# Kernel optimization log

Measured on AMD Instinct MI355X. Metric: run time of the kernel, lower is better.

The kernel has to match this reference:

```python
import jax, jax.numpy as jnp
import numpy as np
import math

N_HEAD = 16
N_EMBD = 1024
HEAD_DIM = N_EMBD // N_HEAD
B, T = 2, 2048


def setup_inputs() -> dict:
    key = jax.random.key(0)
    k1, k2, k3 = jax.random.split(key, 3)
    scale = 0.02
    x = jax.random.normal(k1, (B, T, N_EMBD), dtype=jnp.float32)
    W_attn = jax.random.normal(k2, (N_EMBD, 3 * N_EMBD), dtype=jnp.float32) * scale
    b_attn = jnp.zeros((3 * N_EMBD,), dtype=jnp.float32)
    W_proj = jax.random.normal(k3, (N_EMBD, N_EMBD), dtype=jnp.float32) * scale
    b_proj = jnp.zeros((N_EMBD,), dtype=jnp.float32)
    return {"x": x, "W_attn": W_attn, "b_attn": b_attn, "W_proj": W_proj, "b_proj": b_proj}


def reference(x, W_attn, b_attn, W_proj, b_proj):
    b, t, c = x.shape
    qkv = x @ W_attn + b_attn                      # [B,T,3C]
    q, k, v = jnp.split(qkv, 3, axis=-1)
    # [B,T,C] -> [B,H,T,D]
    def heads(z):
        return z.reshape(b, t, N_HEAD, HEAD_DIM).transpose(0, 2, 1, 3)
    q, k, v = heads(q), heads(k), heads(v)
    att = jnp.einsum('bhqd,bhkd->bhqk', q, k) * (1.0 / math.sqrt(HEAD_DIM))
    causal = jnp.tril(jnp.ones((t, t), dtype=bool))  # [T,T]
    att = jnp.where(causal[None, None], att, -jnp.inf)
    att = jax.nn.softmax(att, axis=-1)
    y = jnp.einsum('bhqk,bhkd->bhqd', att, v)      # [B,H,T,D]
    y = y.transpose(0, 2, 1, 3).reshape(b, t, c)   # [B,T,C]
    return y @ W_proj + b_proj
```

## Files before the change

### kernel.cpp

```cpp
#include <hip/hip_runtime.h>
#include <hip/hip_bf16.h>


typedef __bf16 bf16_t;
typedef __bf16 bf16x8 __attribute__((ext_vector_type(8)));
typedef float f32x4 __attribute__((ext_vector_type(4)));
typedef unsigned short ushort_t;

#define QSCALE 0.18033688011f

__device__ __forceinline__ void glds16(const bf16_t* g, ushort_t* l) {
  __builtin_amdgcn_global_load_lds(
      (const __attribute__((address_space(1))) unsigned int*)g,
      (__attribute__((address_space(3))) unsigned int*)l, 16, 0, 0);
}

__global__ __launch_bounds__(256) void prep_kernel(
    const float* __restrict__ x, const float* __restrict__ W_attn,
    const float* __restrict__ W_proj, ushort_t* __restrict__ Xb,
    ushort_t* __restrict__ WtA, ushort_t* __restrict__ WtP) {
  const int bid = blockIdx.x, tid = threadIdx.x;
  if (bid < 4096) {
    int i = bid * 256 + tid;
    float4 v = ((const float4*)x)[i];
    ushort4 o;
    o.x = __builtin_bit_cast(unsigned short, (bf16_t)v.x);
    o.y = __builtin_bit_cast(unsigned short, (bf16_t)v.y);
    o.z = __builtin_bit_cast(unsigned short, (bf16_t)v.z);
    o.w = __builtin_bit_cast(unsigned short, (bf16_t)v.w);
    ((ushort4*)Xb)[i] = o;
    return;
  }
  __shared__ ushort_t tile[32][33];
  const float* in;
  ushort_t* out;
  int C, bx, by;
  if (bid < 4096 + 3072) { int idx = bid - 4096; in = W_attn; out = WtA; C = 3072; bx = idx % 96; by = idx / 96; }
  else                   { int idx = bid - 7168; in = W_proj; out = WtP; C = 1024; bx = idx % 32; by = idx / 32; }
  const int tx = tid & 31, ty = tid >> 5;
  int cbase = bx * 32, rbase = by * 32;
#pragma unroll
  for (int i = ty; i < 32; i += 8)
    tile[i][tx] = __builtin_bit_cast(
        unsigned short, (bf16_t)in[(size_t)(rbase + i) * C + cbase + tx]);
  __syncthreads();
#pragma unroll
  for (int i = ty; i < 32; i += 8)
    out[(size_t)(cbase + i) * 1024 + rbase + tx] = tile[tx][i];
}

__global__ __launch_bounds__(512) void qkv_gemm_kernel(
    const bf16_t* __restrict__ X, const bf16_t* __restrict__ WtA,
    const float* __restrict__ bias, bf16_t* __restrict__ Qd,
    bf16_t* __restrict__ Kd, bf16_t* __restrict__ Vtd) {
  __shared__ ushort_t As[2 * 256 * 32];
  __shared__ ushort_t Bs[2 * 192 * 32];
  const int tid  = threadIdx.x;
  const int lane = tid & 63, wave = tid >> 6;
  const int l15  = lane & 15, quad = lane >> 4;
  const int wrow = (wave >> 1) * 64;
  const int wcol = (wave & 1) * 96;
  const int mtile = blockIdx.x * 256, ntile = blockIdx.y * 192;
  const int K = 1024;
  const int lr4 = lane >> 2;
  const int csw = ((lane & 3) ^ ((lr4 >> 1) & 3)) * 8;
  const int rsw = (quad ^ ((l15 >> 1) & 3)) * 8;
  const bf16_t* Xrow = X   + (size_t)(mtile + lr4) * K + csw;
  const bf16_t* Wrow = WtA + (size_t)(ntile + lr4) * K + csw;

#define STAGE_QKV(kb, Asl, Bsl)                                              \
  {                                                                          \
    _Pragma("unroll")                                                        \
    for (int kk = 0; kk < 4; kk++) {                                         \
      int s = wave + kk * 8;                                                 \
      if (s < 16)      glds16(Xrow + (size_t)(s * 16) * K + (kb), (Asl) + s * 512); \
      else if (s < 28) glds16(Wrow + (size_t)((s - 16) * 16) * K + (kb), (Bsl) + (s - 16) * 512); \
    }                                                                        \
  }

  f32x4 acc[4][6] = {};
  STAGE_QKV(0, As, Bs);
  __syncthreads();
  for (int kt = 0; kt < 32; kt++) {
    const int cur = kt & 1, nxt = cur ^ 1;
    if (kt + 1 < 32)
      STAGE_QKV((kt + 1) * 32, As + nxt * 8192, Bs + nxt * 6144);
    bf16x8 af[4], bfr[6];
#pragma unroll
    for (int i = 0; i < 4; i++)
      af[i] = *(const bf16x8*)&As[cur * 8192 + (wrow + i * 16 + l15) * 32 + rsw];
#pragma unroll
    for (int j = 0; j < 6; j++)
      bfr[j] = *(const bf16x8*)&Bs[cur * 6144 + (wcol + j * 16 + l15) * 32 + rsw];
#pragma unroll
    for (int i = 0; i < 4; i++)
#pragma unroll
      for (int j = 0; j < 6; j++)
        acc[i][j] = __builtin_amdgcn_mfma_f32_16x16x32_bf16(af[i], bfr[j], acc[i][j], 0, 0, 0);
    __syncthreads();
  }
#undef STAGE_QKV

  const int b = mtile >> 11;
#pragma unroll
  for (int j = 0; j < 6; j++) {
    int n = ntile + wcol + j * 16 + l15;
    float bv = bias[n];
    int sec = n >> 10, cc = n & 1023, h = cc >> 6, d = cc & 63;
    size_t bh = (size_t)(b * 16 + h);
    if (sec == 2) {
#pragma unroll
      for (int i = 0; i < 4; i++) {
        int tperm = (mtile & 2047) + wrow + ((i >> 1) << 5) + (quad << 3) + ((i & 1) << 2);
        ushort4 o4;
        o4.x = __builtin_bit_cast(unsigned short, (bf16_t)(acc[i][j][0] + bv));
        o4.y = __builtin_bit_cast(unsigned short, (bf16_t)(acc[i][j][1] + bv));
        o4.z = __builtin_bit_cast(unsigned short, (bf16_t)(acc[i][j][2] + bv));
        o4.w = __builtin_bit_cast(unsigned short, (bf16_t)(acc[i][j][3] + bv));
        *(ushort4*)&Vtd[(bh * 64 + d) * 2048 + tperm] = o4;
      }
    } else {
      const float sv = (sec == 0) ? QSCALE : 1.0f;
      bf16_t* Od = (sec == 0) ? Qd : Kd;
#pragma unroll
      for (int i = 0; i < 4; i++) {
#pragma unroll
        for (int r = 0; r < 4; r++) {
          int t = (mtile & 2047) + wrow + i * 16 + quad * 4 + r;
          Od[(bh * 2048 + t) * 64 + d] = (bf16_t)((acc[i][j][r] + bv) * sv);
        }
      }
    }
  }
}

__global__ __launch_bounds__(512) void attn_kernel(
    const bf16_t* __restrict__ Q, const bf16_t* __restrict__ K,
    const bf16_t* __restrict__ Vt, bf16_t* __restrict__ Y) {
  __shared__ ushort_t Ks[2][4096];
  __shared__ ushort_t Vs[2][4096];
  const int bh = blockIdx.y;
  const int qt = (blockIdx.y < 16) ? (15 - (int)blockIdx.x) : (int)blockIdx.x;
  const int tid = threadIdx.x, wave = tid >> 6, lane = tid & 63;
  const int l15 = lane & 15, quad = lane >> 4;
  const bf16_t* Qh = Q + (size_t)bh * 2048 * 64;
  const bf16_t* Kh = K + (size_t)bh * 2048 * 64;
  const bf16_t* Vh = Vt + (size_t)bh * 64 * 2048;
  const int b = bh >> 4, h = bh & 15;
  const int qw = qt * 128 + wave * 16;
  const int nkt = 2 * qt + 2;

  bf16x8 qa[2];
#pragma unroll
  for (int kc = 0; kc < 2; kc++)
    qa[kc] = *(const bf16x8*)(Qh + (size_t)(qw + l15) * 64 + kc * 32 + quad * 8);

  f32x4 o[4] = {};
  float lp = 0.f;
  const int rsw = (quad ^ ((l15 >> 1) & 3)) * 8;

  const int lr4 = lane >> 2;
  const int csw = ((lane & 3) ^ ((lr4 >> 1) & 3)) * 8;
  const bool isK = wave < 4;
  const int sw = isK ? wave : wave - 4;
  const int rbase = (sw & 1) * 32;
  const bf16_t* gp0;
  size_t rowstep;
  if (isK) { gp0 = Kh + (size_t)(rbase + lr4) * 64 + (sw >> 1) * 32 + csw;  rowstep = 64; }
  else     { gp0 = Vh + (size_t)(rbase + lr4) * 2048 + (sw >> 1) * 32 + csw; rowstep = 2048; }
  const size_t kstep = isK ? (size_t)64 * 64 : 64;
  ushort_t* dst0 = (isK ? Ks[0] : Vs[0]) + (sw >> 1) * 2048 + rbase * 32;
  ushort_t* dst1 = (isK ? Ks[1] : Vs[1]) + (sw >> 1) * 2048 + rbase * 32;

#pragma unroll
  for (int c = 0; c < 2; c++)
    glds16(gp0 + (size_t)(c * 16) * rowstep, dst0 + c * 512);

  f32x4 zz = {0.f, 0.f, 0.f, 0.f};
  for (int kt = 0; kt < nkt; kt++) {
    const int cur = kt & 1;
    __syncthreads();
    if (kt + 1 < nkt) {
      ushort_t* nd = cur ? dst0 : dst1;
#pragma unroll
      for (int c = 0; c < 2; c++)
        glds16(gp0 + (size_t)(kt + 1) * kstep + (size_t)(c * 16) * rowstep, nd + c * 512);
    }
#pragma unroll
    for (int h32 = 0; h32 < 2; h32++) {
      const int kb32 = kt * 64 + h32 * 32;
      if (kb32 > qw + 15) break;
      bf16x8 kb[2][2];
#pragma unroll
      for (int bn = 0; bn < 2; bn++)
#pragma unroll
        for (int kc = 0; kc < 2; kc++)
          kb[bn][kc] = *(const bf16x8*)&Ks[cur][kc * 2048 + (h32 * 32 + bn * 16 + l15) * 32 + rsw];
      f32x4 s[2];
#pragma unroll
      for (int bn = 0; bn < 2; bn++) {
        f32x4 t0 = __builtin_amdgcn_mfma_f32_16x16x32_bf16(kb[bn][0], qa[0], zz, 0, 0, 0);
        s[bn] = __builtin_amdgcn_mfma_f32_16x16x32_bf16(kb[bn][1], qa[1], t0, 0, 0, 0);
      }
      const bool dg = (kb32 + 31 > qw);
      const int qrow = qw + l15;
      bf16x8 pa;
#pragma unroll
      for (int r = 0; r < 4; r++) {
        float v0 = s[0][r];
        float v1 = s[1][r];
        if (dg) {
          int k0 = kb32 + quad * 4 + r;
          if (k0 > qrow) v0 = -1e5f;
          if (k0 + 16 > qrow) v1 = -1e5f;
        }
        float p0 = __builtin_amdgcn_exp2f(v0);
        float p1 = __builtin_amdgcn_exp2f(v1);
        lp += p0 + p1;
        pa[r]     = (bf16_t)p0;
        pa[4 + r] = (bf16_t)p1;
      }
#pragma unroll
      for (int ns = 0; ns < 4; ns++) {
        bf16x8 vb = *(const bf16x8*)&Vs[cur][h32 * 2048 + (ns * 16 + l15) * 32 + rsw];
        o[ns] = __builtin_amdgcn_mfma_f32_16x16x32_bf16(pa, vb, o[ns], 0, 0, 0);
      }
    }
  }
  lp += __shfl_xor(lp, 16);
  lp += __shfl_xor(lp, 32);
  float inv_l = 1.0f / fmaxf(lp, 1e-30f);
#pragma unroll
  for (int r = 0; r < 4; r++) {
    float il = __shfl(inv_l, quad * 4 + r);
    int t = qw + quad * 4 + r;
#pragma unroll
    for (int ns = 0; ns < 4; ns++) {
      int c = h * 64 + ns * 16 + l15;
      Y[((size_t)(b * 2048 + t)) * 1024 + c] = (bf16_t)(o[ns][r] * il);
    }
  }
}

__global__ __launch_bounds__(256) void proj_gemm_kernel(
    const bf16_t* __restrict__ Yb, const bf16_t* __restrict__ WtP,
    const float* __restrict__ bias, float* __restrict__ out) {
  __shared__ ushort_t As[128 * 32];
  __shared__ ushort_t Bs[64 * 32];
  const int tid = threadIdx.x;
  const int lane = tid & 63, wave = tid >> 6;
  const int l15 = lane & 15, quad = lane >> 4;
  const int wrow = (wave >> 1) * 64, wcol = (wave & 1) * 32;
  const int mtile = blockIdx.x * 128, ntile = blockIdx.y * 64;
  const int K = 1024;
  const int lr = lane >> 2;
  const int lc = (((lane & 3) ^ ((lr >> 1) & 3)) * 8);
  const bf16_t* Ap = Yb + (size_t)(mtile + wave * 32 + lr) * K + lc;
  const bf16_t* Bp = WtP + (size_t)(ntile + wave * 16 + lr) * K + lc;
  const int rsw = (quad ^ ((l15 >> 1) & 3)) * 8;
  ushort_t* Asw = As + wave * 32 * 32;
  ushort_t* Bsw = Bs + wave * 16 * 32;
  f32x4 acc[4][2] = {};
  for (int kb = 0; kb < K; kb += 32) {
    __syncthreads();
    glds16(Ap + kb, Asw);
    glds16(Ap + (size_t)16 * K + kb, Asw + 16 * 32);
    glds16(Bp + kb, Bsw);
    __syncthreads();
    bf16x8 af[4], bfr[2];
#pragma unroll
    for (int i = 0; i < 4; i++)
      af[i] = *(const bf16x8*)&As[(wrow + i * 16 + l15) * 32 + rsw];
#pragma unroll
    for (int j = 0; j < 2; j++)
      bfr[j] = *(const bf16x8*)&Bs[(wcol + j * 16 + l15) * 32 + rsw];
#pragma unroll
    for (int i = 0; i < 4; i++)
#pragma unroll
      for (int j = 0; j < 2; j++)
        acc[i][j] = __builtin_amdgcn_mfma_f32_16x16x32_bf16(af[i], bfr[j], acc[i][j], 0, 0, 0);
  }
#pragma unroll
  for (int j = 0; j < 2; j++) {
    int n = ntile + wcol + j * 16 + l15;
    float bv = bias[n];
#pragma unroll
    for (int i = 0; i < 4; i++) {
#pragma unroll
      for (int r = 0; r < 4; r++) {
        int m = mtile + wrow + i * 16 + quad * 4 + r;
        out[(size_t)m * 1024 + n] = acc[i][j][r] + bv;
      }
    }
  }
}

extern "C" void kernel_launch(void* const* d_in, const int* in_sizes, int n_in,
                              void* d_out, int out_size, void* d_ws, size_t ws_size,
                              hipStream_t stream) {
  const float* x      = (const float*)d_in[0];
  const float* W_attn = (const float*)d_in[1];
  const float* b_attn = (const float*)d_in[2];
  const float* W_proj = (const float*)d_in[3];
  const float* b_proj = (const float*)d_in[4];
  float* out = (float*)d_out;

  bf16_t* ws  = (bf16_t*)d_ws;
  bf16_t* WtA = ws;
  bf16_t* WtP = WtA + (size_t)3072 * 1024;
  bf16_t* Xb  = WtP + (size_t)1024 * 1024;
  bf16_t* Qb  = Xb + (size_t)4194304;
  bf16_t* Kb  = Qb + (size_t)4194304;
  bf16_t* Vtb = Kb + (size_t)4194304;
  bf16_t* Yb  = Vtb + (size_t)4194304;

  prep_kernel<<<8192, 256, 0, stream>>>(x, W_attn, W_proj,
      (ushort_t*)Xb, (ushort_t*)WtA, (ushort_t*)WtP);
  qkv_gemm_kernel<<<dim3(16, 16), 512, 0, stream>>>(Xb, WtA, b_attn, Qb, Kb, Vtb);
  attn_kernel<<<dim3(16, 32), 512, 0, stream>>>(Qb, Kb, Vtb, Yb);
  proj_gemm_kernel<<<dim3(32, 16), 256, 0, stream>>>(Yb, WtP, b_proj, out);
}
```

Before: 173.2 us.

## Triple-buffer QKV GEMM LDS stages with partial vmcnt waits

The QKV projection GEMM moves from double to triple buffering of its LDS tiles, issuing loads two k-steps ahead. Explicit s_waitcnt vmcnt counts per wave replace the full __syncthreads drain, so only the oldest stage must land before each barrier. This should hide global-load latency better, at the cost of 50% more LDS per block, which may reduce occupancy. The hand-counted vmcnt values (4 for waves that issue four loads, 3 for those that issue three) must match exactly for correctness.

```diff
diff --git a/kernel.cpp b/kernel.cpp
--- a/kernel.cpp
+++ b/kernel.cpp
@@ -53,8 +53,8 @@
     const bf16_t* __restrict__ X, const bf16_t* __restrict__ WtA,
     const float* __restrict__ bias, bf16_t* __restrict__ Qd,
     bf16_t* __restrict__ Kd, bf16_t* __restrict__ Vtd) {
-  __shared__ ushort_t As[2 * 256 * 32];
-  __shared__ ushort_t Bs[2 * 192 * 32];
+  __shared__ ushort_t As[3 * 256 * 32];
+  __shared__ ushort_t Bs[3 * 192 * 32];
   const int tid  = threadIdx.x;
   const int lane = tid & 63, wave = tid >> 6;
   const int l15  = lane & 15, quad = lane >> 4;
@@ -68,36 +68,48 @@
   const bf16_t* Xrow = X   + (size_t)(mtile + lr4) * K + csw;
   const bf16_t* Wrow = WtA + (size_t)(ntile + lr4) * K + csw;
 
-#define STAGE_QKV(kb, Asl, Bsl)                                              \
+#define STAGE_QKV(kb, slot)                                                  \
   {                                                                          \
+    ushort_t* Asl = As + (slot) * 8192;                                      \
+    ushort_t* Bsl = Bs + (slot) * 6144;                                      \
     _Pragma("unroll")                                                        \
     for (int kk = 0; kk < 4; kk++) {                                         \
       int s = wave + kk * 8;                                                 \
-      if (s < 16)      glds16(Xrow + (size_t)(s * 16) * K + (kb), (Asl) + s * 512); \
-      else if (s < 28) glds16(Wrow + (size_t)((s - 16) * 16) * K + (kb), (Bsl) + (s - 16) * 512); \
+      if (s < 16)      glds16(Xrow + (size_t)(s * 16) * K + (kb), Asl + s * 512); \
+      else if (s < 28) glds16(Wrow + (size_t)((s - 16) * 16) * K + (kb), Bsl + (s - 16) * 512); \
     }                                                                        \
   }
 
   f32x4 acc[4][6] = {};
-  STAGE_QKV(0, As, Bs);
-  __syncthreads();
-  for (int kt = 0; kt < 32; kt++) {
-    const int cur = kt & 1, nxt = cur ^ 1;
-    if (kt + 1 < 32)
-      STAGE_QKV((kt + 1) * 32, As + nxt * 8192, Bs + nxt * 6144);
+  STAGE_QKV(0, 0);
+  STAGE_QKV(32, 1);
+  if (wave < 4) asm volatile("s_waitcnt vmcnt(4)" ::: "memory");
+  else          asm volatile("s_waitcnt vmcnt(3)" ::: "memory");
+  __builtin_amdgcn_s_barrier();
+  for (int t = 0; t < 32; ++t) {
+    if (t + 2 < 32) STAGE_QKV((t + 2) * 32, (t + 2) % 3);
+    const int curA = (t % 3) * 8192, curB = (t % 3) * 6144;
     bf16x8 af[4], bfr[6];
 #pragma unroll
     for (int i = 0; i < 4; i++)
-      af[i] = *(const bf16x8*)&As[cur * 8192 + (wrow + i * 16 + l15) * 32 + rsw];
+      af[i] = *(const bf16x8*)&As[curA + (wrow + i * 16 + l15) * 32 + rsw];
 #pragma unroll
     for (int j = 0; j < 6; j++)
-      bfr[j] = *(const bf16x8*)&Bs[cur * 6144 + (wcol + j * 16 + l15) * 32 + rsw];
+      bfr[j] = *(const bf16x8*)&Bs[curB + (wcol + j * 16 + l15) * 32 + rsw];
 #pragma unroll
     for (int i = 0; i < 4; i++)
 #pragma unroll
       for (int j = 0; j < 6; j++)
         acc[i][j] = __builtin_amdgcn_mfma_f32_16x16x32_bf16(af[i], bfr[j], acc[i][j], 0, 0, 0);
-    __syncthreads();
+    if (t + 1 < 32) {
+      if (t + 2 < 32) {
+        if (wave < 4) asm volatile("s_waitcnt vmcnt(4) lgkmcnt(0)" ::: "memory");
+        else          asm volatile("s_waitcnt vmcnt(3) lgkmcnt(0)" ::: "memory");
+      } else {
+        asm volatile("s_waitcnt vmcnt(0) lgkmcnt(0)" ::: "memory");
+      }
+      __builtin_amdgcn_s_barrier();
+    }
   }
 #undef STAGE_QKV
 
```

After: 175.6 us. About the same (+1.4%).
